# Performance work log

Hardware: AMD Instinct MI355X
Metric: run time of the kernel (lower is better)

Reference implementation:

```python
import jax, jax.numpy as jnp
import numpy as np

IN_F, HID, OUT_F, N_HEADS, BATCH = 256, 512, 2048, 8, 4096


def _kaiming_uniform(key, shape, fan_in):
    # kaiming_uniform_ with a=sqrt(5): gain = sqrt(2/(1+5)) = 1/sqrt(3)
    gain = 1.0 / np.sqrt(3.0)
    bound = gain * np.sqrt(3.0 / fan_in)  # = sqrt(1/fan_in)
    return jax.random.uniform(key, shape, jnp.float32, -bound, bound)


def setup_inputs() -> dict:
    key = jax.random.key(0)
    kx, ki, k1, k2, k3, k4 = jax.random.split(key, 6)
    X = jax.random.normal(kx, (BATCH, IN_F), jnp.float32)
    X_head_idx = jax.random.randint(ki, (BATCH,), 0, N_HEADS)
    # layer 1: in -> hidden
    W1 = _kaiming_uniform(k1, (N_HEADS, IN_F, HID), IN_F)
    b1 = jax.random.uniform(k2, (N_HEADS, HID), jnp.float32,
                            -1.0 / np.sqrt(IN_F), 1.0 / np.sqrt(IN_F))
    # layer 2: hidden -> out
    W2 = _kaiming_uniform(k3, (N_HEADS, HID, OUT_F), HID)
    b2 = jax.random.uniform(k4, (N_HEADS, OUT_F), jnp.float32,
                            -1.0 / np.sqrt(HID), 1.0 / np.sqrt(HID))
    return {"X": X, "X_head_idx": X_head_idx, "W1": W1, "b1": b1,
            "W2": W2, "b2": b2}


def _selective_linear(x, idx, W, b):
    # x: [B, in], W: [H, in, out], b: [H, out], idx: [B]
    # compute all heads densely, then select each sample's head
    y = jnp.einsum('bi,hio->bho', x, W) + b[None]   # [B, H, out]
    return jnp.take_along_axis(y, idx[:, None, None], axis=1)[:, 0, :]


def reference(X, X_head_idx, W1, b1, W2, b2):
    h = _selective_linear(X, X_head_idx, W1, b1)
    h = jax.nn.relu(h)
    out = _selective_linear(h, X_head_idx, W2, b2)
    return out
```

## Files before the change

kernel.cpp:

```cpp
#include <hip/hip_runtime.h>

#define IN_F 256
#define HID 512
#define OUT_F 2048
#define N_HEADS 8
#define BATCH 4096

typedef __bf16 bf16_t;
typedef bf16_t bf16x8 __attribute__((ext_vector_type(8)));
typedef float f32x4 __attribute__((ext_vector_type(4)));
typedef unsigned short ushort8 __attribute__((ext_vector_type(8)));

typedef __attribute__((address_space(1))) const unsigned int gu32;
typedef __attribute__((address_space(3))) unsigned int lu32;

__device__ inline unsigned short f2bf(float f) {
  union { float f; unsigned u; } v; v.f = f;
  unsigned u = v.u;
  unsigned r = (u + 0x7FFFu + ((u >> 16) & 1u)) >> 16;
  return (unsigned short)r;
}

__device__ inline void transpose64(const float* __restrict__ W,
                                   unsigned short* __restrict__ Wt,
                                   int K, int N, int b, int nt, int kt,
                                   float (*tile)[65]) {
  int per_head = nt * kt;
  int h = b / per_head;
  int rem = b % per_head;
  int n0 = (rem % nt) * 64;
  int k0 = (rem / nt) * 64;
  const float* Wh = W + (size_t)h * K * N;
  unsigned short* Wth = Wt + (size_t)h * K * N;
  int c = threadIdx.x & 63;
  int r0 = threadIdx.x >> 6;
  for (int rr = r0; rr < 64; rr += 4)
    tile[rr][c] = Wh[(size_t)(k0 + rr) * N + n0 + c];
  __syncthreads();
  for (int rr = r0; rr < 64; rr += 4)
    Wth[(size_t)(n0 + rr) * K + k0 + c] = f2bf(tile[c][rr]);
}

__global__ __launch_bounds__(256) void prep_kernel(const int* __restrict__ idx,
                                                   int* __restrict__ order,
                                                   int* __restrict__ offsets,
                                                   const float* __restrict__ W1,
                                                   unsigned short* __restrict__ W1t,
                                                   const float* __restrict__ W2,
                                                   unsigned short* __restrict__ W2t) {
  __shared__ float tile[64][65];
  __shared__ int cnt[N_HEADS];
  __shared__ int base[N_HEADS + 1];
  __shared__ int cur[N_HEADS];
  int b = blockIdx.x;
  if (b == 0) {
    int tid = threadIdx.x;
    if (tid < N_HEADS) cnt[tid] = 0;
    __syncthreads();
    for (int i = tid; i < BATCH; i += 256) atomicAdd(&cnt[idx[i]], 1);
    __syncthreads();
    if (tid == 0) {
      int acc = 0;
      for (int h = 0; h < N_HEADS; ++h) { base[h] = acc; cur[h] = acc; acc += cnt[h]; }
      base[N_HEADS] = acc;
    }
    __syncthreads();
    if (tid < N_HEADS + 1) offsets[tid] = base[tid];
    for (int i = tid; i < BATCH; i += 256) {
      int pos = atomicAdd(&cur[idx[i]], 1);
      order[pos] = i;
    }
  } else if (b < 257) {
    transpose64(W1, W1t, IN_F, HID, b - 1, HID / 64, IN_F / 64, tile);
  } else {
    transpose64(W2, W2t, HID, OUT_F, b - 257, OUT_F / 64, HID / 64, tile);
  }
}

template <int K, int NTOT, int EPI, int GATHER_A>
__global__ __launch_bounds__(256) void gemm_kernel(const unsigned short* __restrict__ A,
                                                   const float* __restrict__ Xf,
                                                   const unsigned short* __restrict__ Wt,
                                                   const float* __restrict__ bias,
                                                   const int* __restrict__ offsets,
                                                   const int* __restrict__ order,
                                                   unsigned short* __restrict__ Hout,
                                                   float* __restrict__ Out) {
  constexpr int BM = 128, BN = 128, BK = 64;
  __shared__ __align__(16) unsigned short As[BM * BK];
  __shared__ __align__(16) unsigned short Bs[BN * BK];

  int my = blockIdx.y;
  int head = -1, row0 = 0, rows = 0, acc_t = 0;
#pragma unroll
  for (int h = 0; h < N_HEADS; ++h) {
    int o0 = offsets[h], o1 = offsets[h + 1];
    int cnt = o1 - o0;
    int t = (cnt + BM - 1) / BM;
    if (head < 0 && my < acc_t + t) {
      head = h;
      int lt = my - acc_t;
      row0 = o0 + lt * BM;
      rows = min(BM, cnt - lt * BM);
    }
    acc_t += t;
  }
  if (head < 0) return;

  int n0 = blockIdx.x * BN;
  const unsigned short* Bh = Wt + (size_t)head * (size_t)NTOT * K;

  int tid = threadIdx.x;
  int wave = tid >> 6;
  int lane = tid & 63;
  int q = lane >> 4;
  int l16 = lane & 15;
  int w_m = wave >> 1, w_n = wave & 1;

  int srow = lane >> 3;
  int seg = lane & 7;
  int segl = seg ^ srow;

  const unsigned short* bptr[4];
#pragma unroll
  for (int i = 0; i < 4; ++i) {
    int rl = wave * 32 + i * 8 + srow;
    bptr[i] = Bh + (size_t)(n0 + rl) * K + segl * 8;
  }

  const unsigned short* aptr[4];
  const float* gptr[4];
#pragma unroll
  for (int i = 0; i < 4; ++i) {
    int rl = wave * 32 + i * 8 + srow;
    int pr = row0 + min(rl, rows - 1);
    if (GATHER_A) {
      gptr[i] = Xf + (size_t)order[pr] * K + segl * 8;
      aptr[i] = nullptr;
    } else {
      aptr[i] = A + (size_t)pr * K + segl * 8;
      gptr[i] = nullptr;
    }
  }

  f32x4 acc[4][4];
#pragma unroll
  for (int i = 0; i < 4; ++i)
#pragma unroll
    for (int j = 0; j < 4; ++j) acc[i][j] = (f32x4){0.f, 0.f, 0.f, 0.f};

  for (int k0 = 0; k0 < K; k0 += BK) {
#pragma unroll
    for (int i = 0; i < 4; ++i) {
      __builtin_amdgcn_global_load_lds((gu32*)bptr[i], (lu32*)(Bs + wave * 2048 + i * 512), 16, 0, 0);
      bptr[i] += BK;
    }
    if (GATHER_A == 0) {
#pragma unroll
      for (int i = 0; i < 4; ++i) {
        __builtin_amdgcn_global_load_lds((gu32*)aptr[i], (lu32*)(As + wave * 2048 + i * 512), 16, 0, 0);
        aptr[i] += BK;
      }
    } else {
#pragma unroll
      for (int i = 0; i < 4; ++i) {
        float4 v0 = *(const float4*)(gptr[i]);
        float4 v1 = *(const float4*)(gptr[i] + 4);
        gptr[i] += BK;
        ushort8 o;
        o[0] = f2bf(v0.x); o[1] = f2bf(v0.y); o[2] = f2bf(v0.z); o[3] = f2bf(v0.w);
        o[4] = f2bf(v1.x); o[5] = f2bf(v1.y); o[6] = f2bf(v1.z); o[7] = f2bf(v1.w);
        int rl = wave * 32 + i * 8 + srow;
        *(ushort8*)(As + rl * 64 + seg * 8) = o;
      }
    }
    __syncthreads();

#pragma unroll
    for (int kk = 0; kk < 2; ++kk) {
      bf16x8 af[4], bfr[4];
#pragma unroll
      for (int i = 0; i < 4; ++i) {
        int ra = w_m * 64 + i * 16 + l16;
        int rb = w_n * 64 + i * 16 + l16;
        int ps = ((kk * 4 + q) ^ (l16 & 7)) * 8;
        af[i] = *(const bf16x8*)(As + ra * 64 + ps);
        bfr[i] = *(const bf16x8*)(Bs + rb * 64 + ps);
      }
#pragma unroll
      for (int mi = 0; mi < 4; ++mi)
#pragma unroll
        for (int ni = 0; ni < 4; ++ni)
          acc[mi][ni] = __builtin_amdgcn_mfma_f32_16x16x32_bf16(af[mi], bfr[ni], acc[mi][ni], 0, 0, 0);
    }
    __syncthreads();
  }

  float bval[4];
#pragma unroll
  for (int ni = 0; ni < 4; ++ni)
    bval[ni] = bias[(size_t)head * NTOT + n0 + w_n * 64 + ni * 16 + l16];

#pragma unroll
  for (int mi = 0; mi < 4; ++mi) {
#pragma unroll
    for (int r = 0; r < 4; ++r) {
      int m = w_m * 64 + mi * 16 + q * 4 + r;
      if (m < rows) {
        int p = row0 + m;
        if (EPI == 0) {
#pragma unroll
          for (int ni = 0; ni < 4; ++ni) {
            int n = n0 + w_n * 64 + ni * 16 + l16;
            float v = acc[mi][ni][r] + bval[ni];
            v = v > 0.f ? v : 0.f;
            Hout[(size_t)p * NTOT + n] = f2bf(v);
          }
        } else {
          int rg = order[p];
#pragma unroll
          for (int ni = 0; ni < 4; ++ni) {
            int n = n0 + w_n * 64 + ni * 16 + l16;
            Out[(size_t)rg * NTOT + n] = acc[mi][ni][r] + bval[ni];
          }
        }
      }
    }
  }
}

extern "C" void kernel_launch(void* const* d_in, const int* in_sizes, int n_in,
                              void* d_out, int out_size, void* d_ws, size_t ws_size,
                              hipStream_t stream) {
  const float* X = (const float*)d_in[0];
  const int* idxh = (const int*)d_in[1];
  const float* W1 = (const float*)d_in[2];
  const float* b1 = (const float*)d_in[3];
  const float* W2 = (const float*)d_in[4];
  const float* b2 = (const float*)d_in[5];
  float* out = (float*)d_out;

  char* ws = (char*)d_ws;
  int* order = (int*)ws;                     ws += (size_t)BATCH * 4;
  int* offsets = (int*)ws;                   ws += 64;
  unsigned short* W1t = (unsigned short*)ws; ws += (size_t)N_HEADS * IN_F * HID * 2;
  unsigned short* W2t = (unsigned short*)ws; ws += (size_t)N_HEADS * HID * OUT_F * 2;
  unsigned short* Hb = (unsigned short*)ws;  ws += (size_t)BATCH * HID * 2;

  prep_kernel<<<dim3(2305), dim3(256), 0, stream>>>(idxh, order, offsets, W1, W1t, W2, W2t);

  constexpr int MT = BATCH / 128 + N_HEADS;
  gemm_kernel<IN_F, HID, 0, 1><<<dim3(HID / 128, MT), dim3(256), 0, stream>>>(
      nullptr, X, W1t, b1, offsets, order, Hb, nullptr);
  gemm_kernel<HID, OUT_F, 1, 0><<<dim3(OUT_F / 128, MT), dim3(256), 0, stream>>>(
      Hb, nullptr, W2t, b2, offsets, order, nullptr, out);
}
```

Baseline: 140.6 us.

## Overlap W2 transpose with first GEMM and double-buffer second GEMM

Result: no change. 138.8 us (-1.3%).

```diff
diff --git a/kernel.cpp b/kernel.cpp
--- a/kernel.cpp
+++ b/kernel.cpp
@@ -34,20 +34,28 @@
   unsigned short* Wth = Wt + (size_t)h * K * N;
   int c = threadIdx.x & 63;
   int r0 = threadIdx.x >> 6;
+#pragma unroll
   for (int rr = r0; rr < 64; rr += 4)
     tile[rr][c] = Wh[(size_t)(k0 + rr) * N + n0 + c];
   __syncthreads();
-  for (int rr = r0; rr < 64; rr += 4)
-    Wth[(size_t)(n0 + rr) * K + k0 + c] = f2bf(tile[c][rr]);
-}
-
-__global__ __launch_bounds__(256) void prep_kernel(const int* __restrict__ idx,
-                                                   int* __restrict__ order,
-                                                   int* __restrict__ offsets,
-                                                   const float* __restrict__ W1,
-                                                   unsigned short* __restrict__ W1t,
-                                                   const float* __restrict__ W2,
-                                                   unsigned short* __restrict__ W2t) {
+  int c4 = threadIdx.x & 15;
+  int r1 = threadIdx.x >> 4;
+#pragma unroll
+  for (int rr = r1; rr < 64; rr += 16) {
+    ushort4 o;
+    o.x = f2bf(tile[c4 * 4 + 0][rr]);
+    o.y = f2bf(tile[c4 * 4 + 1][rr]);
+    o.z = f2bf(tile[c4 * 4 + 2][rr]);
+    o.w = f2bf(tile[c4 * 4 + 3][rr]);
+    *(ushort4*)&Wth[(size_t)(n0 + rr) * K + k0 + c4 * 4] = o;
+  }
+}
+
+__global__ __launch_bounds__(256) void k1_kernel(const int* __restrict__ idx,
+                                                 int* __restrict__ order,
+                                                 int* __restrict__ offsets,
+                                                 const float* __restrict__ W1,
+                                                 unsigned short* __restrict__ W1t) {
   __shared__ float tile[64][65];
   __shared__ int cnt[N_HEADS];
   __shared__ int base[N_HEADS + 1];
@@ -57,7 +65,15 @@
     int tid = threadIdx.x;
     if (tid < N_HEADS) cnt[tid] = 0;
     __syncthreads();
-    for (int i = tid; i < BATCH; i += 256) atomicAdd(&cnt[idx[i]], 1);
+    const int4* idx4 = (const int4*)idx;
+    int4 v[4];
+#pragma unroll
+    for (int i = 0; i < 4; ++i) v[i] = idx4[tid + i * 256];
+#pragma unroll
+    for (int i = 0; i < 4; ++i) {
+      atomicAdd(&cnt[v[i].x], 1); atomicAdd(&cnt[v[i].y], 1);
+      atomicAdd(&cnt[v[i].z], 1); atomicAdd(&cnt[v[i].w], 1);
+    }
     __syncthreads();
     if (tid == 0) {
       int acc = 0;
@@ -66,48 +82,51 @@
     }
     __syncthreads();
     if (tid < N_HEADS + 1) offsets[tid] = base[tid];
-    for (int i = tid; i < BATCH; i += 256) {
-      int pos = atomicAdd(&cur[idx[i]], 1);
-      order[pos] = i;
-    }
-  } else if (b < 257) {
+#pragma unroll
+    for (int i = 0; i < 4; ++i) {
+      int i0 = (tid + i * 256) * 4;
+      order[atomicAdd(&cur[v[i].x], 1)] = i0;
+      order[atomicAdd(&cur[v[i].y], 1)] = i0 + 1;
+      order[atomicAdd(&cur[v[i].z], 1)] = i0 + 2;
+      order[atomicAdd(&cur[v[i].w], 1)] = i0 + 3;
+    }
+  } else {
     transpose64(W1, W1t, IN_F, HID, b - 1, HID / 64, IN_F / 64, tile);
-  } else {
-    transpose64(W2, W2t, HID, OUT_F, b - 257, OUT_F / 64, HID / 64, tile);
-  }
-}
-
-template <int K, int NTOT, int EPI, int GATHER_A>
-__global__ __launch_bounds__(256) void gemm_kernel(const unsigned short* __restrict__ A,
-                                                   const float* __restrict__ Xf,
-                                                   const unsigned short* __restrict__ Wt,
-                                                   const float* __restrict__ bias,
-                                                   const int* __restrict__ offsets,
-                                                   const int* __restrict__ order,
-                                                   unsigned short* __restrict__ Hout,
-                                                   float* __restrict__ Out) {
-  constexpr int BM = 128, BN = 128, BK = 64;
-  __shared__ __align__(16) unsigned short As[BM * BK];
-  __shared__ __align__(16) unsigned short Bs[BN * BK];
-
-  int my = blockIdx.y;
-  int head = -1, row0 = 0, rows = 0, acc_t = 0;
+  }
+}
+
+__device__ inline bool resolve_head(const int* __restrict__ offsets, int my,
+                                    int& head, int& row0, int& rows) {
+  head = -1; row0 = 0; rows = 0;
+  int acc_t = 0;
 #pragma unroll
   for (int h = 0; h < N_HEADS; ++h) {
     int o0 = offsets[h], o1 = offsets[h + 1];
     int cnt = o1 - o0;
-    int t = (cnt + BM - 1) / BM;
+    int t = (cnt + 127) / 128;
     if (head < 0 && my < acc_t + t) {
       head = h;
       int lt = my - acc_t;
-      row0 = o0 + lt * BM;
-      rows = min(BM, cnt - lt * BM);
+      row0 = o0 + lt * 128;
+      rows = min(128, cnt - lt * 128);
     }
     acc_t += t;
   }
-  if (head < 0) return;
-
-  int n0 = blockIdx.x * BN;
+  return head >= 0;
+}
+
+__device__ void gemm1_body(const float* __restrict__ Xf,
+                           const unsigned short* __restrict__ Wt,
+                           const float* __restrict__ bias,
+                           const int* __restrict__ offsets,
+                           const int* __restrict__ order,
+                           unsigned short* __restrict__ Hout,
+                           unsigned short* As, unsigned short* Bs,
+                           int bx, int my) {
+  constexpr int K = IN_F, NTOT = HID, BK = 64, NT = K / BK;
+  int head, row0, rows;
+  if (!resolve_head(offsets, my, head, row0, rows)) return;
+  int n0 = bx * 128;
   const unsigned short* Bh = Wt + (size_t)head * (size_t)NTOT * K;
 
   int tid = threadIdx.x;
@@ -122,25 +141,13 @@
   int segl = seg ^ srow;
 
   const unsigned short* bptr[4];
+  const float* gptr[4];
 #pragma unroll
   for (int i = 0; i < 4; ++i) {
     int rl = wave * 32 + i * 8 + srow;
     bptr[i] = Bh + (size_t)(n0 + rl) * K + segl * 8;
-  }
-
-  const unsigned short* aptr[4];
-  const float* gptr[4];
-#pragma unroll
-  for (int i = 0; i < 4; ++i) {
-    int rl = wave * 32 + i * 8 + srow;
     int pr = row0 + min(rl, rows - 1);
-    if (GATHER_A) {
-      gptr[i] = Xf + (size_t)order[pr] * K + segl * 8;
-      aptr[i] = nullptr;
-    } else {
-      aptr[i] = A + (size_t)pr * K + segl * 8;
-      gptr[i] = nullptr;
-    }
+    gptr[i] = Xf + (size_t)order[pr] * K + segl * 8;
   }
 
   f32x4 acc[4][4];
@@ -149,43 +156,33 @@
 #pragma unroll
     for (int j = 0; j < 4; ++j) acc[i][j] = (f32x4){0.f, 0.f, 0.f, 0.f};
 
-  for (int k0 = 0; k0 < K; k0 += BK) {
+#pragma unroll
+  for (int t = 0; t < NT; ++t) {
 #pragma unroll
     for (int i = 0; i < 4; ++i) {
       __builtin_amdgcn_global_load_lds((gu32*)bptr[i], (lu32*)(Bs + wave * 2048 + i * 512), 16, 0, 0);
       bptr[i] += BK;
     }
-    if (GATHER_A == 0) {
-#pragma unroll
-      for (int i = 0; i < 4; ++i) {
-        __builtin_amdgcn_global_load_lds((gu32*)aptr[i], (lu32*)(As + wave * 2048 + i * 512), 16, 0, 0);
-        aptr[i] += BK;
-      }
-    } else {
-#pragma unroll
-      for (int i = 0; i < 4; ++i) {
-        float4 v0 = *(const float4*)(gptr[i]);
-        float4 v1 = *(const float4*)(gptr[i] + 4);
-        gptr[i] += BK;
-        ushort8 o;
-        o[0] = f2bf(v0.x); o[1] = f2bf(v0.y); o[2] = f2bf(v0.z); o[3] = f2bf(v0.w);
-        o[4] = f2bf(v1.x); o[5] = f2bf(v1.y); o[6] = f2bf(v1.z); o[7] = f2bf(v1.w);
-        int rl = wave * 32 + i * 8 + srow;
-        *(ushort8*)(As + rl * 64 + seg * 8) = o;
-      }
-    }
-    __syncthreads();
-
+#pragma unroll
+    for (int i = 0; i < 4; ++i) {
+      float4 v0 = *(const float4*)(gptr[i]);
+      float4 v1 = *(const float4*)(gptr[i] + 4);
+      gptr[i] += BK;
+      ushort8 o;
+      o[0] = f2bf(v0.x); o[1] = f2bf(v0.y); o[2] = f2bf(v0.z); o[3] = f2bf(v0.w);
+      o[4] = f2bf(v1.x); o[5] = f2bf(v1.y); o[6] = f2bf(v1.z); o[7] = f2bf(v1.w);
+      int rl = wave * 32 + i * 8 + srow;
+      *(ushort8*)(As + rl * 64 + seg * 8) = o;
+    }
+    __syncthreads();
 #pragma unroll
     for (int kk = 0; kk < 2; ++kk) {
       bf16x8 af[4], bfr[4];
 #pragma unroll
       for (int i = 0; i < 4; ++i) {
-        int ra = w_m * 64 + i * 16 + l16;
-        int rb = w_n * 64 + i * 16 + l16;
         int ps = ((kk * 4 + q) ^ (l16 & 7)) * 8;
-        af[i] = *(const bf16x8*)(As + ra * 64 + ps);
-        bfr[i] = *(const bf16x8*)(Bs + rb * 64 + ps);
+        af[i] = *(const bf16x8*)(As + (w_m * 64 + i * 16 + l16) * 64 + ps);
+        bfr[i] = *(const bf16x8*)(Bs + (w_n * 64 + i * 16 + l16) * 64 + ps);
       }
 #pragma unroll
       for (int mi = 0; mi < 4; ++mi)
@@ -208,21 +205,136 @@
       int m = w_m * 64 + mi * 16 + q * 4 + r;
       if (m < rows) {
         int p = row0 + m;
-        if (EPI == 0) {
-#pragma unroll
-          for (int ni = 0; ni < 4; ++ni) {
-            int n = n0 + w_n * 64 + ni * 16 + l16;
-            float v = acc[mi][ni][r] + bval[ni];
-            v = v > 0.f ? v : 0.f;
-            Hout[(size_t)p * NTOT + n] = f2bf(v);
-          }
-        } else {
-          int rg = order[p];
-#pragma unroll
-          for (int ni = 0; ni < 4; ++ni) {
-            int n = n0 + w_n * 64 + ni * 16 + l16;
-            Out[(size_t)rg * NTOT + n] = acc[mi][ni][r] + bval[ni];
-          }
+#pragma unroll
+        for (int ni = 0; ni < 4; ++ni) {
+          int n = n0 + w_n * 64 + ni * 16 + l16;
+          float v = acc[mi][ni][r] + bval[ni];
+          v = v > 0.f ? v : 0.f;
+          Hout[(size_t)p * NTOT + n] = f2bf(v);
+        }
+      }
+    }
+  }
+}
+
+__global__ __launch_bounds__(256) void k2_kernel(const float* __restrict__ X,
+                                                 const int* __restrict__ order,
+                                                 const int* __restrict__ offsets,
+                                                 const unsigned short* __restrict__ W1t,
+                                                 const float* __restrict__ b1,
+                                                 unsigned short* __restrict__ Hb,
+                                                 const float* __restrict__ W2,
+                                                 unsigned short* __restrict__ W2t) {
+  __shared__ __align__(16) unsigned char smem[32768];
+  int b = blockIdx.x;
+  if (b < 160) {
+    gemm1_body(X, W1t, b1, offsets, order, Hb,
+               (unsigned short*)smem, (unsigned short*)(smem + 16384),
+               b & 3, b >> 2);
+  } else {
+    transpose64(W2, W2t, HID, OUT_F, b - 160, OUT_F / 64, HID / 64,
+                (float(*)[65])smem);
+  }
+}
+
+__global__ __launch_bounds__(256) void gemm2_kernel(const unsigned short* __restrict__ A,
+                                                    const unsigned short* __restrict__ Wt,
+                                                    const float* __restrict__ bias,
+                                                    const int* __restrict__ offsets,
+                                                    const int* __restrict__ order,
+                                                    float* __restrict__ Out) {
+  constexpr int K = HID, NTOT = OUT_F, BK = 64, NT = K / BK;
+  __shared__ __align__(16) unsigned short As[2][128 * BK];
+  __shared__ __align__(16) unsigned short Bs[2][128 * BK];
+
+  int head, row0, rows;
+  if (!resolve_head(offsets, blockIdx.y, head, row0, rows)) return;
+  int n0 = blockIdx.x * 128;
+  const unsigned short* Bh = Wt + (size_t)head * (size_t)NTOT * K;
+
+  int tid = threadIdx.x;
+  int wave = tid >> 6;
+  int lane = tid & 63;
+  int q = lane >> 4;
+  int l16 = lane & 15;
+  int w_m = wave >> 1, w_n = wave & 1;
+
+  int srow = lane >> 3;
+  int seg = lane & 7;
+  int segl = seg ^ srow;
+
+  const unsigned short* aptr[4];
+  const unsigned short* bptr[4];
+#pragma unroll
+  for (int i = 0; i < 4; ++i) {
+    int rl = wave * 32 + i * 8 + srow;
+    bptr[i] = Bh + (size_t)(n0 + rl) * K + segl * 8;
+    int pr = row0 + min(rl, rows - 1);
+    aptr[i] = A + (size_t)pr * K + segl * 8;
+  }
+
+  f32x4 acc[4][4];
+#pragma unroll
+  for (int i = 0; i < 4; ++i)
+#pragma unroll
+    for (int j = 0; j < 4; ++j) acc[i][j] = (f32x4){0.f, 0.f, 0.f, 0.f};
+
+#pragma unroll
+  for (int i = 0; i < 4; ++i) {
+    __builtin_amdgcn_global_load_lds((gu32*)bptr[i], (lu32*)(&Bs[0][wave * 2048 + i * 512]), 16, 0, 0);
+    bptr[i] += BK;
+    __builtin_amdgcn_global_load_lds((gu32*)aptr[i], (lu32*)(&As[0][wave * 2048 + i * 512]), 16, 0, 0);
+    aptr[i] += BK;
+  }
+  __syncthreads();
+
+  int cur = 0;
+#pragma unroll
+  for (int t = 0; t < NT; ++t) {
+    if (t + 1 < NT) {
+#pragma unroll
+      for (int i = 0; i < 4; ++i) {
+        __builtin_amdgcn_global_load_lds((gu32*)bptr[i], (lu32*)(&Bs[cur ^ 1][wave * 2048 + i * 512]), 16, 0, 0);
+        bptr[i] += BK;
+        __builtin_amdgcn_global_load_lds((gu32*)aptr[i], (lu32*)(&As[cur ^ 1][wave * 2048 + i * 512]), 16, 0, 0);
+        aptr[i] += BK;
+      }
+    }
+#pragma unroll
+    for (int kk = 0; kk < 2; ++kk) {
+      bf16x8 af[4], bfr[4];
+#pragma unroll
+      for (int i = 0; i < 4; ++i) {
+        int ps = ((kk * 4 + q) ^ (l16 & 7)) * 8;
+        af[i] = *(const bf16x8*)(&As[cur][(w_m * 64 + i * 16 + l16) * 64 + ps]);
+        bfr[i] = *(const bf16x8*)(&Bs[cur][(w_n * 64 + i * 16 + l16) * 64 + ps]);
+      }
+#pragma unroll
+      for (int mi = 0; mi < 4; ++mi)
+#pragma unroll
+        for (int ni = 0; ni < 4; ++ni)
+          acc[mi][ni] = __builtin_amdgcn_mfma_f32_16x16x32_bf16(af[mi], bfr[ni], acc[mi][ni], 0, 0, 0);
+    }
+    __syncthreads();
+    cur ^= 1;
+  }
+
+  float bval[4];
+#pragma unroll
+  for (int ni = 0; ni < 4; ++ni)
+    bval[ni] = bias[(size_t)head * NTOT + n0 + w_n * 64 + ni * 16 + l16];
+
+#pragma unroll
+  for (int mi = 0; mi < 4; ++mi) {
+#pragma unroll
+    for (int r = 0; r < 4; ++r) {
+      int m = w_m * 64 + mi * 16 + q * 4 + r;
+      if (m < rows) {
+        int rg = order[row0 + m];
+#pragma unroll
+        for (int ni = 0; ni < 4; ++ni) {
+          int n = n0 + w_n * 64 + ni * 16 + l16;
+          Out[(size_t)rg * NTOT + n] = acc[mi][ni][r] + bval[ni];
         }
       }
     }
@@ -247,11 +359,10 @@
   unsigned short* W2t = (unsigned short*)ws; ws += (size_t)N_HEADS * HID * OUT_F * 2;
   unsigned short* Hb = (unsigned short*)ws;  ws += (size_t)BATCH * HID * 2;
 
-  prep_kernel<<<dim3(2305), dim3(256), 0, stream>>>(idxh, order, offsets, W1, W1t, W2, W2t);
+  k1_kernel<<<dim3(257), dim3(256), 0, stream>>>(idxh, order, offsets, W1, W1t);
+  k2_kernel<<<dim3(2208), dim3(256), 0, stream>>>(X, order, offsets, W1t, b1, Hb, W2, W2t);
 
   constexpr int MT = BATCH / 128 + N_HEADS;
-  gemm_kernel<IN_F, HID, 0, 1><<<dim3(HID / 128, MT), dim3(256), 0, stream>>>(
-      nullptr, X, W1t, b1, offsets, order, Hb, nullptr);
-  gemm_kernel<HID, OUT_F, 1, 0><<<dim3(OUT_F / 128, MT), dim3(256), 0, stream>>>(
-      Hb, nullptr, W2t, b2, offsets, order, nullptr, out);
-}
+  gemm2_kernel<<<dim3(OUT_F / 128, MT), dim3(256), 0, stream>>>(
+      Hb, W2t, b2, offsets, order, out);
+}
```
